# Kernel tuning notes

Measured on AMD Instinct MI355X. Metric: run time of the kernel, lower is better.

The kernel has to match this reference:

```python
import jax, jax.numpy as jnp
import numpy as np

HEAD_DIM = 128
BITS = 4
N_LEVELS = 2 ** BITS  # 16


def _make_codebook(d, n_levels):
    # Lloyd-Max-style codebook for coordinates of rotated unit vectors.
    # Coordinate distribution ~ N(0, 1/d) for large d; centroids at mid-quantiles,
    # decision boundaries at centroid midpoints, clipped to [-1, 1].
    probs = (np.arange(n_levels) + 0.5) / n_levels
    c = np.asarray(jax.scipy.stats.norm.ppf(probs)) / np.sqrt(d)
    c = np.clip(c, -0.999, 0.999)
    mids = (c[1:] + c[:-1]) / 2.0
    boundaries = np.concatenate([[-1.0], mids, [1.0]])  # len n_levels+1
    return c.astype(np.float32), boundaries.astype(np.float32)


def setup_inputs() -> dict:
    key = jax.random.key(0)
    d = HEAD_DIM
    # orthogonal rotation via QR with sign fix (matches generate_rotation_matrix)
    rng = np.random.default_rng(42)
    G = rng.standard_normal((d, d)).astype(np.float32)
    Q, R = np.linalg.qr(G)
    s = np.sign(np.diag(R))
    s[s == 0] = 1.0
    Pi = jnp.asarray(Q * s[None, :], dtype=jnp.float32)
    cen, bnd = _make_codebook(d, N_LEVELS)
    centroids = jnp.asarray(cen)
    boundaries = jnp.asarray(bnd)
    x = jax.random.normal(key, (4, 32, 2048, d), dtype=jnp.float32)
    return {"x": x, "Pi": Pi, "centroids": centroids, "boundaries": boundaries}


def reference(x, Pi, centroids, boundaries):
    d = x.shape[-1]
    flat = x.reshape(-1, d).astype(jnp.float32)          # (N, d)
    norms = jnp.sqrt(jnp.sum(flat * flat, axis=-1, keepdims=True))  # (N, 1)
    x_unit = flat / (norms + 1e-8)
    rotated = x_unit @ Pi.T                               # (N, d)
    # per-coordinate Lloyd-Max bucketize over interior boundaries
    idx = jnp.searchsorted(boundaries[1:-1], rotated).astype(jnp.uint8)
    values = centroids[idx.astype(jnp.int32)]             # (N, d) codebook gather
    # norms stored as fp16 then upcast (matches norm_dtype=float16 round trip)
    norms_q = norms[:, 0].astype(jnp.float16).astype(jnp.float32)
    recon = (values @ Pi) * norms_q[:, None]              # un-rotate + rescale
    return recon.reshape(x.shape)
```

## Files before the change

kernel.cpp:

```cpp
#include <hip/hip_runtime.h>
#include <hip/hip_fp16.h>

#define HD 128

#define RCHK 1.5e-5f
#define EPS 1.5e-7
#define DMG_GATE 0.095f

#define SWX(r, c4) ((c4) ^ (((r) ^ ((r) >> 3)) & 7))

using frag_ab = __attribute__((ext_vector_type(8))) short;
using frag_cd = __attribute__((ext_vector_type(4))) float;

__device__ __forceinline__ unsigned short bf16rn(float f) {
  unsigned u = __float_as_uint(f);
  return (unsigned short)((u + 0x7fffu + ((u >> 16) & 1u)) >> 16);
}
__device__ __forceinline__ void bsplit(float f, unsigned short& h,
                                       unsigned short& l) {
  h = bf16rn(f);
  l = bf16rn(f - __uint_as_float(((unsigned)h) << 16));
}

__device__ __noinline__ unsigned rareRefine(
    const float* __restrict__ xr, const float* __restrict__ prG,
    const float* __restrict__ centroids, const float* __restrict__ boundaries,
    float inv, float nf, unsigned* flag)
{
  double a = 0.0;
  for (int k = 0; k < HD; ++k) {
    float xk = xr[k] * inv;
    a = fma((double)xk, (double)prG[k], a);
  }
  unsigned idx = 0;
  for (int t = 0; t < 15; ++t) idx += ((double)boundaries[t + 1] < a) ? 1u : 0u;
  int tt = -1;
  if      (fabs(a - (double)boundaries[1])  < EPS) tt = 0;
  else if (fabs(a - (double)boundaries[2])  < EPS) tt = 1;
  else if (fabs(a - (double)boundaries[3])  < EPS) tt = 2;
  else if (fabs(a - (double)boundaries[13]) < EPS) tt = 12;
  else if (fabs(a - (double)boundaries[14]) < EPS) tt = 13;
  else if (fabs(a - (double)boundaries[15]) < EPS) tt = 14;
  if (tt >= 0) {
    float maxp = 0.f;
    for (int k = 0; k < HD; ++k) maxp = fmaxf(maxp, fabsf(prG[k]));
    float half = 0.5f * (centroids[tt + 1] - centroids[tt]);
    if (half * maxp * nf <= DMG_GATE) { idx = (unsigned)tt; *flag = 1u; }
  }
  return idx;
}

__global__ void tq_prep(const float* __restrict__ Pi,
                        unsigned short* __restrict__ ws)
{
  int e = blockIdx.x * 256 + threadIdx.x;
  int j = e >> 7, k = e & 127;
  unsigned short h, l;
  bsplit(Pi[e], h, l);
  size_t b1 = (size_t)(k >> 5) * 16384 +
              (size_t)(((k >> 3) & 3) << 11) + j * 16 + (k & 7) * 2;
  ws[b1 >> 1] = h;
  ws[(b1 + 8192) >> 1] = l;
  size_t b2 = 65536 + (size_t)(j >> 5) * 16384 +
              (size_t)(((j >> 3) & 3) << 11) + k * 16 + (j & 7) * 2;
  ws[b2 >> 1] = h;
  ws[(b2 + 8192) >> 1] = l;
}

#define ABYTE(pl, r, k) \
  ((pl) * 16384 + (((k) >> 3) << 10) + ((r) << 4) + (((k) & 7) << 1))

__global__ __launch_bounds__(256, 3) void tq_fused(
    const float* __restrict__ x, const float* __restrict__ Pi,
    const float* __restrict__ centroids, const float* __restrict__ boundaries,
    const char* __restrict__ wsb, float* __restrict__ out, int n_rows)
{
  __shared__ int4 sMain4[2048];
  __shared__ int4 sPB4[1024];
  __shared__ float sInv[64], sNf[64], sNq[64];
  __shared__ float sCen[16];
  __shared__ unsigned sCenHL[16];

  char*  sA  = (char*)sMain4;
  float* sXf = (float*)sMain4;
  char*  sB  = (char*)sPB4;

  const int t = threadIdx.x;
  const int row0 = blockIdx.x * 64;
  if (t < 16) {
    float c = centroids[t];
    sCen[t] = c;
    unsigned short hh, ll;
    bsplit(c, hh, ll);
    sCenHL[t] = (unsigned)hh | ((unsigned)ll << 16);
  }

#pragma unroll 1
  for (int it = 0; it < 8; ++it) {
    int idx = t + 256 * it;
    int r = idx >> 5, c4 = idx & 31;
    int gr = row0 + r; if (gr >= n_rows) gr = n_rows - 1;
    float4 v = ((const float4*)(x + (size_t)gr * HD))[c4];
    ((float4*)sXf)[r * 32 + SWX(r, c4)] = v;
  }
  __syncthreads();

  if (t < 64) {
    const int r = t;
    double ss = 0.0;
#pragma unroll 1
    for (int c4 = 0; c4 < 32; ++c4) {
      float4 v = ((const float4*)sXf)[r * 32 + SWX(r, c4)];
      ss = fma((double)v.x, (double)v.x, ss);
      ss = fma((double)v.y, (double)v.y, ss);
      ss = fma((double)v.z, (double)v.z, ss);
      ss = fma((double)v.w, (double)v.w, ss);
    }
    double nrm = sqrt(ss);
    float nf = (float)nrm;
    float inv = (float)(1.0 / (nrm + 1e-8));
    sInv[r] = inv; sNf[r] = nf;
    sNq[r] = __half2float(__float2half(nf));
#pragma unroll 1
    for (int c4 = 0; c4 < 32; ++c4) {
      float4* p = ((float4*)sXf) + r * 32 + SWX(r, c4);
      float4 v = *p;
      v.x *= inv; v.y *= inv; v.z *= inv; v.w *= inv;
      *p = v;
    }
  }
  __syncthreads();

  {
    const int r = t >> 2, q = t & 3;
    float v[32];
#pragma unroll
    for (int i = 0; i < 8; ++i) {
      float4 f = ((const float4*)sXf)[r * 32 + SWX(r, q * 8 + i)];
      v[4 * i + 0] = f.x; v[4 * i + 1] = f.y;
      v[4 * i + 2] = f.z; v[4 * i + 3] = f.w;
    }
    __syncthreads();
#pragma unroll
    for (int sq = 0; sq < 4; ++sq) {
      unsigned hw[4], lw[4];
#pragma unroll
      for (int p = 0; p < 4; ++p) {
        unsigned short h0, l0, h1, l1;
        bsplit(v[sq * 8 + 2 * p + 0], h0, l0);
        bsplit(v[sq * 8 + 2 * p + 1], h1, l1);
        hw[p] = (unsigned)h0 | ((unsigned)h1 << 16);
        lw[p] = (unsigned)l0 | ((unsigned)l1 << 16);
      }
      int slot = q * 4 + sq;
      *(int4*)(sA + (slot << 10) + (r << 4)) =
          make_int4(hw[0], hw[1], hw[2], hw[3]);
      *(int4*)(sA + 16384 + (slot << 10) + (r << 4)) =
          make_int4(lw[0], lw[1], lw[2], lw[3]);
    }
  }

  const int wave = t >> 6;
  const int g = (t >> 4) & 3;
  const int m = t & 15;
  const int rowb = wave * 16;

  frag_cd acc[8];
#pragma unroll
  for (int ct = 0; ct < 8; ++ct) acc[ct] = (frag_cd){0.f, 0.f, 0.f, 0.f};

  {
    int4 p0[4];
#pragma unroll
    for (int i = 0; i < 4; ++i)
      p0[i] = ((const int4*)wsb)[t + 256 * i];
#pragma unroll
    for (int i = 0; i < 4; ++i) sPB4[t + 256 * i] = p0[i];
  }
  __syncthreads();

#pragma unroll 1
  for (int ch = 0; ch < 4; ++ch) {
    frag_ab ah, al, bbh[8], bbl[8];
    ah = *(const frag_ab*)(sA + ((ch * 4 + g) << 10) + ((rowb + m) << 4));
    al = *(const frag_ab*)(sA + 16384 + ((ch * 4 + g) << 10) + ((rowb + m) << 4));
#pragma unroll
    for (int ct = 0; ct < 8; ++ct)
      bbh[ct] = *(const frag_ab*)(sB + (g << 11) + ((ct * 16 + m) << 4));
    int4 pf[4];
    if (ch < 3) {
#pragma unroll
      for (int i = 0; i < 4; ++i)
        pf[i] = ((const int4*)(wsb + (size_t)(ch + 1) * 16384))[t + 256 * i];
    }
#pragma unroll
    for (int ct = 0; ct < 8; ++ct)
      acc[ct] = __builtin_amdgcn_mfma_f32_16x16x32_bf16(ah, bbh[ct], acc[ct],
                                                        0, 0, 0);
#pragma unroll
    for (int ct = 0; ct < 8; ++ct)
      acc[ct] = __builtin_amdgcn_mfma_f32_16x16x32_bf16(al, bbh[ct], acc[ct],
                                                        0, 0, 0);
#pragma unroll
    for (int ct = 0; ct < 8; ++ct)
      bbl[ct] = *(const frag_ab*)(sB + 8192 + (g << 11) + ((ct * 16 + m) << 4));
#pragma unroll
    for (int ct = 0; ct < 8; ++ct)
      acc[ct] = __builtin_amdgcn_mfma_f32_16x16x32_bf16(ah, bbl[ct], acc[ct],
                                                        0, 0, 0);
    if (ch < 3) {
      __syncthreads();
#pragma unroll
      for (int i = 0; i < 4; ++i) sPB4[t + 256 * i] = pf[i];
      __syncthreads();
    }
  }

  unsigned nearmask = 0u;
  {
    float bnd[15];
#pragma unroll
    for (int b = 0; b < 15; ++b) bnd[b] = boundaries[b + 1];
#pragma unroll
    for (int ct = 0; ct < 8; ++ct)
#pragma unroll
      for (int rg = 0; rg < 4; ++rg) {
        float v = acc[ct][rg];
        int rl = rowb + g * 4 + rg;
        int j = ct * 16 + m;
        unsigned idx = 0u;
#pragma unroll
        for (int b = 0; b < 15; ++b) idx += (bnd[b] < v) ? 1u : 0u;
        bool nr = (fabsf(v - bnd[0])  < RCHK) | (fabsf(v - bnd[1])  < RCHK) |
                  (fabsf(v - bnd[2])  < RCHK) | (fabsf(v - bnd[12]) < RCHK) |
                  (fabsf(v - bnd[13]) < RCHK) | (fabsf(v - bnd[14]) < RCHK);
        if (__builtin_expect((int)(nr && (row0 + rl) < n_rows), 0))
          nearmask |= 1u << (ct * 4 + rg);
        unsigned hl = sCenHL[idx];
        *(unsigned short*)(sA + ABYTE(0, rl, j)) = (unsigned short)hl;
        *(unsigned short*)(sA + ABYTE(1, rl, j)) = (unsigned short)(hl >> 16);
      }

    while (__builtin_expect(nearmask != 0u, 0)) {
      int b = __builtin_ctz(nearmask);
      nearmask &= nearmask - 1;
      int ct = b >> 2, rg = b & 3;
      int rl = rowb + g * 4 + rg;
      int j = ct * 16 + m;
      int gr = row0 + rl;
      unsigned fl = 0u;
      unsigned idx = rareRefine(x + (size_t)gr * HD, Pi + (size_t)j * HD,
                                centroids, boundaries, sInv[rl], sNf[rl], &fl);
      float val = sCen[idx];
      if (fl) val = 0.5f * (val + sCen[idx + 1]);
      unsigned short hh, ll;
      bsplit(val, hh, ll);
      *(unsigned short*)(sA + ABYTE(0, rl, j)) = hh;
      *(unsigned short*)(sA + ABYTE(1, rl, j)) = ll;
    }
  }

  frag_cd ac2[8];
#pragma unroll
  for (int kt = 0; kt < 8; ++kt) ac2[kt] = (frag_cd){0.f, 0.f, 0.f, 0.f};

  __syncthreads();
  {
    int4 p0[4];
#pragma unroll
    for (int i = 0; i < 4; ++i)
      p0[i] = ((const int4*)(wsb + 65536))[t + 256 * i];
#pragma unroll
    for (int i = 0; i < 4; ++i) sPB4[t + 256 * i] = p0[i];
  }
  __syncthreads();

#pragma unroll 1
  for (int jc = 0; jc < 4; ++jc) {
    frag_ab ah, al, bbh[8], bbl[8];
    ah = *(const frag_ab*)(sA + ((jc * 4 + g) << 10) + ((rowb + m) << 4));
    al = *(const frag_ab*)(sA + 16384 + ((jc * 4 + g) << 10) + ((rowb + m) << 4));
#pragma unroll
    for (int kt = 0; kt < 8; ++kt)
      bbh[kt] = *(const frag_ab*)(sB + (g << 11) + ((kt * 16 + m) << 4));
    int4 pf[4];
    if (jc < 3) {
#pragma unroll
      for (int i = 0; i < 4; ++i)
        pf[i] = ((const int4*)(wsb + 65536 + (size_t)(jc + 1) * 16384))
                    [t + 256 * i];
    }
#pragma unroll
    for (int kt = 0; kt < 8; ++kt)
      ac2[kt] = __builtin_amdgcn_mfma_f32_16x16x32_bf16(ah, bbh[kt], ac2[kt],
                                                        0, 0, 0);
#pragma unroll
    for (int kt = 0; kt < 8; ++kt)
      ac2[kt] = __builtin_amdgcn_mfma_f32_16x16x32_bf16(al, bbh[kt], ac2[kt],
                                                        0, 0, 0);
#pragma unroll
    for (int kt = 0; kt < 8; ++kt)
      bbl[kt] = *(const frag_ab*)(sB + 8192 + (g << 11) + ((kt * 16 + m) << 4));
#pragma unroll
    for (int kt = 0; kt < 8; ++kt)
      ac2[kt] = __builtin_amdgcn_mfma_f32_16x16x32_bf16(ah, bbl[kt], ac2[kt],
                                                        0, 0, 0);
    if (jc < 3) {
      __syncthreads();
#pragma unroll
      for (int i = 0; i < 4; ++i) sPB4[t + 256 * i] = pf[i];
      __syncthreads();
    }
  }

#pragma unroll
  for (int kt = 0; kt < 8; ++kt)
#pragma unroll
    for (int rg = 0; rg < 4; ++rg) {
      int rl = rowb + g * 4 + rg;
      int gr = row0 + rl;
      if (gr < n_rows)
        out[(size_t)gr * HD + kt * 16 + m] = ac2[kt][rg] * sNq[rl];
    }
}

extern "C" void kernel_launch(void* const* d_in, const int* in_sizes, int n_in,
                              void* d_out, int out_size, void* d_ws, size_t ws_size,
                              hipStream_t stream) {
  const float* x   = (const float*)d_in[0];
  const float* Pi  = (const float*)d_in[1];
  const float* cen = (const float*)d_in[2];
  const float* bnd = (const float*)d_in[3];
  float* out = (float*)d_out;

  int n_rows = in_sizes[0] / HD;
  int blocks = (n_rows + 63) / 64;

  tq_prep<<<64, 256, 0, stream>>>(Pi, (unsigned short*)d_ws);
  tq_fused<<<blocks, 256, 0, stream>>>(x, Pi, cen, bnd, (const char*)d_ws,
                                       out, n_rows);
}
```

Baseline: 427.5 us.

## Restructure Pi chunk staging: early first-chunk load, drop in-loop prefetch registers

Moves the first Pi chunk load to the kernel start so it overlaps the x load and normalization. The second GEMM's first chunk is now fetched before the bucketize phase to hide its latency. The per-iteration register prefetch of later chunks is replaced by loads issued after a barrier, which lowers register pressure but exposes global latency inside the loop. Launch bounds drop from 3 to 2 blocks per SM, giving the compiler more registers at the cost of possible occupancy.

Result: faster. 372.8 us (-12.8%).

```diff
diff --git a/kernel.cpp b/kernel.cpp
--- a/kernel.cpp
+++ b/kernel.cpp
@@ -70,7 +70,7 @@
 #define ABYTE(pl, r, k) \
   ((pl) * 16384 + (((k) >> 3) << 10) + ((r) << 4) + (((k) & 7) << 1))
 
-__global__ __launch_bounds__(256, 3) void tq_fused(
+__global__ __launch_bounds__(256, 2) void tq_fused(
     const float* __restrict__ x, const float* __restrict__ Pi,
     const float* __restrict__ centroids, const float* __restrict__ boundaries,
     const char* __restrict__ wsb, float* __restrict__ out, int n_rows)
@@ -87,6 +87,14 @@
 
   const int t = threadIdx.x;
   const int row0 = blockIdx.x * 64;
+
+  {
+    int4 c0[4];
+#pragma unroll
+    for (int i = 0; i < 4; ++i) c0[i] = ((const int4*)wsb)[t + 256 * i];
+#pragma unroll
+    for (int i = 0; i < 4; ++i) sPB4[t + 256 * i] = c0[i];
+  }
   if (t < 16) {
     float c = centroids[t];
     sCen[t] = c;
@@ -159,6 +167,7 @@
           make_int4(lw[0], lw[1], lw[2], lw[3]);
     }
   }
+  __syncthreads();
 
   const int wave = t >> 6;
   const int g = (t >> 4) & 3;
@@ -169,16 +178,6 @@
 #pragma unroll
   for (int ct = 0; ct < 8; ++ct) acc[ct] = (frag_cd){0.f, 0.f, 0.f, 0.f};
 
-  {
-    int4 p0[4];
-#pragma unroll
-    for (int i = 0; i < 4; ++i)
-      p0[i] = ((const int4*)wsb)[t + 256 * i];
-#pragma unroll
-    for (int i = 0; i < 4; ++i) sPB4[t + 256 * i] = p0[i];
-  }
-  __syncthreads();
-
 #pragma unroll 1
   for (int ch = 0; ch < 4; ++ch) {
     frag_ab ah, al, bbh[8], bbl[8];
@@ -187,34 +186,37 @@
 #pragma unroll
     for (int ct = 0; ct < 8; ++ct)
       bbh[ct] = *(const frag_ab*)(sB + (g << 11) + ((ct * 16 + m) << 4));
-    int4 pf[4];
+#pragma unroll
+    for (int ct = 0; ct < 8; ++ct)
+      acc[ct] = __builtin_amdgcn_mfma_f32_16x16x32_bf16(ah, bbh[ct], acc[ct],
+                                                        0, 0, 0);
+#pragma unroll
+    for (int ct = 0; ct < 8; ++ct)
+      acc[ct] = __builtin_amdgcn_mfma_f32_16x16x32_bf16(al, bbh[ct], acc[ct],
+                                                        0, 0, 0);
+#pragma unroll
+    for (int ct = 0; ct < 8; ++ct)
+      bbl[ct] = *(const frag_ab*)(sB + 8192 + (g << 11) + ((ct * 16 + m) << 4));
+#pragma unroll
+    for (int ct = 0; ct < 8; ++ct)
+      acc[ct] = __builtin_amdgcn_mfma_f32_16x16x32_bf16(ah, bbl[ct], acc[ct],
+                                                        0, 0, 0);
+    __syncthreads();
     if (ch < 3) {
+      int4 nb[4];
 #pragma unroll
       for (int i = 0; i < 4; ++i)
-        pf[i] = ((const int4*)(wsb + (size_t)(ch + 1) * 16384))[t + 256 * i];
-    }
-#pragma unroll
-    for (int ct = 0; ct < 8; ++ct)
-      acc[ct] = __builtin_amdgcn_mfma_f32_16x16x32_bf16(ah, bbh[ct], acc[ct],
-                                                        0, 0, 0);
-#pragma unroll
-    for (int ct = 0; ct < 8; ++ct)
-      acc[ct] = __builtin_amdgcn_mfma_f32_16x16x32_bf16(al, bbh[ct], acc[ct],
-                                                        0, 0, 0);
-#pragma unroll
-    for (int ct = 0; ct < 8; ++ct)
-      bbl[ct] = *(const frag_ab*)(sB + 8192 + (g << 11) + ((ct * 16 + m) << 4));
-#pragma unroll
-    for (int ct = 0; ct < 8; ++ct)
-      acc[ct] = __builtin_amdgcn_mfma_f32_16x16x32_bf16(ah, bbl[ct], acc[ct],
-                                                        0, 0, 0);
-    if (ch < 3) {
+        nb[i] = ((const int4*)(wsb + (size_t)(ch + 1) * 16384))[t + 256 * i];
+#pragma unroll
+      for (int i = 0; i < 4; ++i) sPB4[t + 256 * i] = nb[i];
       __syncthreads();
-#pragma unroll
-      for (int i = 0; i < 4; ++i) sPB4[t + 256 * i] = pf[i];
-      __syncthreads();
-    }
-  }
+    }
+  }
+
+  int4 e0[4];
+#pragma unroll
+  for (int i = 0; i < 4; ++i)
+    e0[i] = ((const int4*)(wsb + 65536))[t + 256 * i];
 
   unsigned nearmask = 0u;
   {
@@ -260,20 +262,13 @@
     }
   }
 
+#pragma unroll
+  for (int i = 0; i < 4; ++i) sPB4[t + 256 * i] = e0[i];
+  __syncthreads();
+
   frag_cd ac2[8];
 #pragma unroll
   for (int kt = 0; kt < 8; ++kt) ac2[kt] = (frag_cd){0.f, 0.f, 0.f, 0.f};
-
-  __syncthreads();
-  {
-    int4 p0[4];
-#pragma unroll
-    for (int i = 0; i < 4; ++i)
-      p0[i] = ((const int4*)(wsb + 65536))[t + 256 * i];
-#pragma unroll
-    for (int i = 0; i < 4; ++i) sPB4[t + 256 * i] = p0[i];
-  }
-  __syncthreads();
 
 #pragma unroll 1
   for (int jc = 0; jc < 4; ++jc) {
@@ -283,13 +278,6 @@
 #pragma unroll
     for (int kt = 0; kt < 8; ++kt)
       bbh[kt] = *(const frag_ab*)(sB + (g << 11) + ((kt * 16 + m) << 4));
-    int4 pf[4];
-    if (jc < 3) {
-#pragma unroll
-      for (int i = 0; i < 4; ++i)
-        pf[i] = ((const int4*)(wsb + 65536 + (size_t)(jc + 1) * 16384))
-                    [t + 256 * i];
-    }
 #pragma unroll
     for (int kt = 0; kt < 8; ++kt)
       ac2[kt] = __builtin_amdgcn_mfma_f32_16x16x32_bf16(ah, bbh[kt], ac2[kt],
@@ -307,8 +295,13 @@
                                                         0, 0, 0);
     if (jc < 3) {
       __syncthreads();
-#pragma unroll
-      for (int i = 0; i < 4; ++i) sPB4[t + 256 * i] = pf[i];
+      int4 nb[4];
+#pragma unroll
+      for (int i = 0; i < 4; ++i)
+        nb[i] = ((const int4*)(wsb + 65536 + (size_t)(jc + 1) * 16384))
+                    [t + 256 * i];
+#pragma unroll
+      for (int i = 0; i < 4; ++i) sPB4[t + 256 * i] = nb[i];
       __syncthreads();
     }
   }
```
